# Kernel optimization log

Hardware: AMD Instinct MI355X
Metric: run time of the kernel (lower is better)

Reference implementation:

```python
import jax, jax.numpy as jnp
import numpy as np

B, L, D = 16, 1024, 512
EPS = 1e-6


def setup_inputs() -> dict:
    key = jax.random.key(0)
    ks = jax.random.split(key, 12)
    inp = {
        'q': jax.random.normal(ks[0], (B, L, D), jnp.float32),
        'k': jax.random.normal(ks[1], (B, L, D), jnp.float32),
        'v': jax.random.normal(ks[2], (B, L, D), jnp.float32),
        'inputs_lengths': jax.random.randint(ks[3], (B,), 1, L + 1),
        'distance_matrix': jax.random.uniform(ks[4], (B, L, L), jnp.float32),
        'Wq': jax.random.normal(ks[5], (D, D), jnp.float32) / np.sqrt(D),
        'Wk': jax.random.normal(ks[6], (D, D), jnp.float32) / np.sqrt(D),
        'Wv': jax.random.normal(ks[7], (D, D), jnp.float32) / np.sqrt(D),
        'Wqt': jax.random.normal(ks[8], (D, D), jnp.float32) / np.sqrt(D),
        'Wkt': jax.random.normal(ks[9], (D, D), jnp.float32) / np.sqrt(D),
        'Wfc': jax.random.normal(ks[10], (D, D), jnp.float32) / np.sqrt(D),
        'gamma': jnp.ones((D,), jnp.float32),
        'beta': jnp.zeros((D,), jnp.float32),
    }
    return inp


def reference(q, k, v, inputs_lengths, distance_matrix, Wq, Wk, Wv, Wqt, Wkt, Wfc, gamma, beta):
    temperature = jnp.asarray(D, q.dtype) ** 0.5
    residual = q
    # projections (torch Linear: x @ W.T)
    qp = jnp.einsum('bld,ed->ble', q, Wq)
    kp = jnp.einsum('bld,ed->ble', k, Wk)
    vp = jnp.einsum('bld,ed->ble', v, Wv)
    qt = jnp.einsum('bld,ed->ble', q, Wqt)
    kt = jnp.einsum('bld,ed->ble', k, Wkt)
    # distance-weighted time features: [B,L,L] @ [B,L,D]
    qt = jnp.einsum('blm,bmd->bld', distance_matrix, qt)
    kt = jnp.einsum('blm,bmd->bld', distance_matrix, kt)
    # scores: content + distance term
    attn = jnp.einsum('bld,bmd->blm', qp / temperature, kp)
    attn = attn + jnp.einsum('bld,bmd->blm', qt / temperature, kt)
    # pad_zero_masking: zero out key positions beyond each sequence length
    mask = (jnp.arange(L)[None, :] < inputs_lengths[:, None]).astype(attn.dtype)  # [B, L]
    mask = mask[:, None, :]  # [B, 1, L] broadcast over query dim
    attn = jnp.tanh(attn * mask) * mask
    out = jnp.einsum('blm,bmd->bld', attn, vp)
    out = jnp.einsum('bld,ed->ble', out, Wfc) + residual
    # LayerNorm(eps=1e-6)
    mu = jnp.mean(out, axis=-1, keepdims=True)
    var = jnp.mean((out - mu) ** 2, axis=-1, keepdims=True)
    out = (out - mu) * jax.lax.rsqrt(var + EPS) * gamma + beta
    return (out, attn)
```

## Files before the change

kernel.cpp:

```cpp
#include <hip/hip_runtime.h>
#include <math.h>

#define LL 1024
#define DD 512
#define NB 16

typedef __attribute__((ext_vector_type(8))) short bf16x8;
typedef __attribute__((ext_vector_type(4))) float f32x4;
typedef unsigned short u16;
typedef unsigned int u32;
typedef const __attribute__((address_space(1))) void* gptr_t;
typedef __attribute__((address_space(3))) void* sptr_t;

static const long NLD = (long)NB * LL * DD;
static const long NLL = (long)NB * LL * LL;

__device__ __forceinline__ u16 f2bf(float x) {
  u32 u = __float_as_uint(x);
  u += 0x7fffu + ((u >> 16) & 1u);
  return (u16)(u >> 16);
}
__device__ __forceinline__ float bf2f(u16 h) {
  return __uint_as_float((u32)h << 16);
}

__device__ __forceinline__ int xcd_chunk16(int flat) {
  const int j = flat >> 3;
  return ((j >> 4) << 7) + ((flat & 7) << 4) + (j & 15);
}

__global__ __launch_bounds__(256) void k_split3(
    const float* __restrict__ q, const float* __restrict__ k,
    const float* __restrict__ v, u16* __restrict__ qh, u16* __restrict__ ql,
    u16* __restrict__ kh, u16* __restrict__ kl, u16* __restrict__ vh) {
  const int z = blockIdx.z;
  const float* x = (z == 0) ? q : (z == 1) ? k : v;
  u16* hi = (z == 0) ? qh : (z == 1) ? kh : vh;
  u16* lo = (z == 0) ? ql : kl;
  const long stride = (long)gridDim.x * 1024;
  for (long i = ((long)blockIdx.x * 256 + threadIdx.x) * 4; i < NLD;
       i += stride) {
    const float4 vv = *(const float4*)(x + i);
    ushort4 h;
    h.x = f2bf(vv.x);
    h.y = f2bf(vv.y);
    h.z = f2bf(vv.z);
    h.w = f2bf(vv.w);
    *(ushort4*)(hi + i) = h;
    if (z < 2) {
      ushort4 s;
      s.x = f2bf(vv.x - bf2f(h.x));
      s.y = f2bf(vv.y - bf2f(h.y));
      s.z = f2bf(vv.z - bf2f(h.z));
      s.w = f2bf(vv.w - bf2f(h.w));
      *(ushort4*)(lo + i) = s;
    }
  }
}

__global__ __launch_bounds__(256) void k_splitd(const float* __restrict__ x,
                                                u16* __restrict__ hi,
                                                u16* __restrict__ lo) {
  const long stride = (long)gridDim.x * 1024;
  for (long i = ((long)blockIdx.x * 256 + threadIdx.x) * 4; i < NLL;
       i += stride) {
    const float4 v = *(const float4*)(x + i);
    ushort4 h, s;
    h.x = f2bf(v.x);
    h.y = f2bf(v.y);
    h.z = f2bf(v.z);
    h.w = f2bf(v.w);
    s.x = f2bf(v.x - bf2f(h.x));
    s.y = f2bf(v.y - bf2f(h.y));
    s.z = f2bf(v.z - bf2f(h.z));
    s.w = f2bf(v.w - bf2f(h.w));
    *(ushort4*)(hi + i) = h;
    *(ushort4*)(lo + i) = s;
  }
}

__global__ __launch_bounds__(256) void k_splitw(
    const float* __restrict__ Wq, const float* __restrict__ Wk,
    const float* __restrict__ Wv, const float* __restrict__ Wfc,
    const float* __restrict__ Wqt, const float* __restrict__ Wkt,
    u16* __restrict__ Wq_h, u16* __restrict__ Wk_h, u16* __restrict__ Wv_h,
    u16* __restrict__ Wfc_h, u16* __restrict__ Wqt_h,
    u16* __restrict__ Wqt_l, u16* __restrict__ Wkt_h,
    u16* __restrict__ Wkt_l) {
  const int z = blockIdx.z;
  const float* x;
  u16 *hi, *lo = nullptr;
  switch (z) {
    case 0: x = Wq; hi = Wq_h; break;
    case 1: x = Wk; hi = Wk_h; break;
    case 2: x = Wv; hi = Wv_h; break;
    case 3: x = Wfc; hi = Wfc_h; break;
    case 4: x = Wqt; hi = Wqt_h; lo = Wqt_l; break;
    default: x = Wkt; hi = Wkt_h; lo = Wkt_l; break;
  }
  const long i = ((long)blockIdx.x * 256 + threadIdx.x) * 4;
  const float4 v = *(const float4*)(x + i);
  ushort4 h;
  h.x = f2bf(v.x);
  h.y = f2bf(v.y);
  h.z = f2bf(v.z);
  h.w = f2bf(v.w);
  *(ushort4*)(hi + i) = h;
  if (z >= 4) {
    ushort4 s;
    s.x = f2bf(v.x - bf2f(h.x));
    s.y = f2bf(v.y - bf2f(h.y));
    s.z = f2bf(v.z - bf2f(h.z));
    s.w = f2bf(v.w - bf2f(h.w));
    *(ushort4*)(lo + i) = s;
  }
}

template <int NISS>
__device__ __forceinline__ void stage_tile(const u16* __restrict__ G, long ld,
                                           int row0, int k0, char* lds, int w,
                                           int l) {
#pragma unroll
  for (int i = 0; i < NISS; ++i) {
    const int off = i * 4096 + w * 1024 + l * 16;
    const int r = off >> 6;
    const int cp = (off >> 4) & 3;
    const int c = cp ^ ((r >> 1) & 3);
    __builtin_amdgcn_global_load_lds(
        (gptr_t)(G + (long)(row0 + r) * ld + k0 + c * 8),
        (sptr_t)(lds + i * 4096 + w * 1024), 16, 0, 0);
  }
}

__device__ __forceinline__ bf16x8 read_frag(const char* lds, int r, int ks) {
  const int cp = ks ^ ((r >> 1) & 3);
  return *(const bf16x8*)(lds + r * 64 + cp * 16);
}

__device__ __forceinline__ void core_plain(const u16* __restrict__ A, long lda,
                                           const u16* __restrict__ B, long ldb,
                                           int K, int bm, int bn, char* smem,
                                           f32x4 acc[4][4]) {
  const int tid = threadIdx.x, w = tid >> 6, l = tid & 63;
  const int wm = (w >> 1) * 64, wn = (w & 1) * 64;
  const int fr = l & 15, ks = l >> 4;
  char* As = smem;
  char* Bs = smem + 8192;
  for (int k0 = 0; k0 < K; k0 += 32) {
    stage_tile<2>(A, lda, bm, k0, As, w, l);
    stage_tile<2>(B, ldb, bn, k0, Bs, w, l);
    __syncthreads();
    bf16x8 af[4], bg[4];
#pragma unroll
    for (int i = 0; i < 4; ++i) {
      af[i] = read_frag(As, wm + i * 16 + fr, ks);
      bg[i] = read_frag(Bs, wn + i * 16 + fr, ks);
    }
#pragma unroll
    for (int mi = 0; mi < 4; ++mi)
#pragma unroll
      for (int ni = 0; ni < 4; ++ni)
        acc[mi][ni] = __builtin_amdgcn_mfma_f32_16x16x32_bf16(
            af[mi], bg[ni], acc[mi][ni], 0, 0, 0);
    __syncthreads();
  }
}

__device__ __forceinline__ void core_split(
    const u16* __restrict__ Ah, const u16* __restrict__ Al, long lda,
    const u16* __restrict__ Bh, const u16* __restrict__ Bl, long ldb, int K,
    int bm, int bn, char* smem, f32x4 acc[4][4]) {
  const int tid = threadIdx.x, w = tid >> 6, l = tid & 63;
  const int wm = (w >> 1) * 64, wn = (w & 1) * 64;
  const int fr = l & 15, ks = l >> 4;
  char* Ash = smem;
  char* Bsh = smem + 8192;
  char* Asl = smem + 16384;
  char* Bsl = smem + 24576;
  for (int k0 = 0; k0 < K; k0 += 32) {
    stage_tile<2>(Ah, lda, bm, k0, Ash, w, l);
    stage_tile<2>(Bh, ldb, bn, k0, Bsh, w, l);
    stage_tile<2>(Al, lda, bm, k0, Asl, w, l);
    stage_tile<2>(Bl, ldb, bn, k0, Bsl, w, l);
    __syncthreads();
    bf16x8 ah[4], bh[4];
#pragma unroll
    for (int i = 0; i < 4; ++i) {
      ah[i] = read_frag(Ash, wm + i * 16 + fr, ks);
      bh[i] = read_frag(Bsh, wn + i * 16 + fr, ks);
    }
#pragma unroll
    for (int mi = 0; mi < 4; ++mi)
#pragma unroll
      for (int ni = 0; ni < 4; ++ni)
        acc[mi][ni] = __builtin_amdgcn_mfma_f32_16x16x32_bf16(
            ah[mi], bh[ni], acc[mi][ni], 0, 0, 0);
    bf16x8 bl[4];
#pragma unroll
    for (int ni = 0; ni < 4; ++ni)
      bl[ni] = read_frag(Bsl, wn + ni * 16 + fr, ks);
#pragma unroll
    for (int mi = 0; mi < 4; ++mi)
#pragma unroll
      for (int ni = 0; ni < 4; ++ni)
        acc[mi][ni] = __builtin_amdgcn_mfma_f32_16x16x32_bf16(
            ah[mi], bl[ni], acc[mi][ni], 0, 0, 0);
    bf16x8 al[4];
#pragma unroll
    for (int mi = 0; mi < 4; ++mi)
      al[mi] = read_frag(Asl, wm + mi * 16 + fr, ks);
#pragma unroll
    for (int mi = 0; mi < 4; ++mi)
#pragma unroll
      for (int ni = 0; ni < 4; ++ni)
        acc[mi][ni] = __builtin_amdgcn_mfma_f32_16x16x32_bf16(
            al[mi], bh[ni], acc[mi][ni], 0, 0, 0);
    __syncthreads();
  }
}

#define EPI_PROLOG()                                       \
  const int tid = threadIdx.x, w = tid >> 6, l = tid & 63; \
  const int wm = (w >> 1) * 64, wn = (w & 1) * 64;         \
  const int fr = l & 15, ks = l >> 4;

__device__ __forceinline__ int scan_batches(const int* __restrict__ lens,
                                            int e, int mult, int* loc,
                                            int* rem) {
  for (int i = 0; i < NB; ++i) {
    const int c = mult * ((lens[i] + 127) >> 7);
    if (e < c) {
      *loc = e;
      return i;
    }
    e -= c;
  }
  *rem = e;
  return -1;
}

__global__ __launch_bounds__(256, 3) void k_proj_p(
    const u16* __restrict__ q_hi, const u16* __restrict__ k_hi,
    const u16* __restrict__ v_hi, const u16* __restrict__ Wq_h,
    const u16* __restrict__ Wk_h, const u16* __restrict__ Wv_h,
    const int* __restrict__ lens, u16* __restrict__ qp, u16* __restrict__ kp,
    u16* __restrict__ vp) {
  const int flat = xcd_chunk16(blockIdx.x);
  const u16 *A, *B;
  u16* C;
  int bm, bn;
  if (flat < 512) {
    A = q_hi;
    B = Wq_h;
    C = qp;
    bm = (flat >> 2) * 128;
    bn = (flat & 3) * 128;
  } else {
    int loc, rem;
    int b = scan_batches(lens, flat - 512, 4, &loc, &rem);
    if (b >= 0) {
      A = k_hi;
      B = Wk_h;
      C = kp;
    } else {
      b = scan_batches(lens, rem, 4, &loc, &rem);
      if (b < 0) return;
      A = v_hi;
      B = Wv_h;
      C = vp;
    }
    bm = b * 1024 + (loc >> 2) * 128;
    bn = (loc & 3) * 128;
  }
  __shared__ __align__(16) char smem[16384];
  f32x4 acc[4][4] = {};
  core_plain(A, DD, B, DD, DD, bm, bn, smem, acc);
  EPI_PROLOG()
#pragma unroll
  for (int mi = 0; mi < 4; ++mi) {
    const int R0 = bm + wm + mi * 16 + ks * 4;
#pragma unroll
    for (int ni = 0; ni < 4; ++ni) {
      const int col = bn + wn + ni * 16 + fr;
#pragma unroll
      for (int j = 0; j < 4; ++j)
        C[(long)(R0 + j) * DD + col] = f2bf(acc[mi][ni][j]);
    }
  }
}

__global__ __launch_bounds__(256, 2) void k_proj_t(
    const u16* __restrict__ q_hi, const u16* __restrict__ q_lo,
    const u16* __restrict__ k_hi, const u16* __restrict__ k_lo,
    const u16* __restrict__ Wqt_h, const u16* __restrict__ Wqt_l,
    const u16* __restrict__ Wkt_h, const u16* __restrict__ Wkt_l,
    u16* __restrict__ qT_h, u16* __restrict__ qT_l, u16* __restrict__ kT_h,
    u16* __restrict__ kT_l) {
  const int sel = blockIdx.z;
  const u16* Ah = sel ? k_hi : q_hi;
  const u16* Al = sel ? k_lo : q_lo;
  const u16* Bh = sel ? Wkt_h : Wqt_h;
  const u16* Bl = sel ? Wkt_l : Wqt_l;
  u16* Ch = sel ? kT_h : qT_h;
  u16* Cl = sel ? kT_l : qT_l;
  __shared__ __align__(16) char smem[32768];
  const int bm = blockIdx.y * 128, bn = blockIdx.x * 128;
  f32x4 acc[4][4] = {};
  core_split(Ah, Al, DD, Bh, Bl, DD, DD, bm, bn, smem, acc);
  EPI_PROLOG()
  u16* tb = (u16*)smem;
  const int b = bm >> 10, lr0 = bm & 1023;
  for (int part = 0; part < 2; ++part) {
    u16* OT = part ? Cl : Ch;
    for (int half = 0; half < 2; ++half) {
      __syncthreads();
      if ((wn >> 6) == half) {
#pragma unroll
        for (int mi = 0; mi < 4; ++mi) {
          const int rloc = wm + mi * 16 + ks * 4;
#pragma unroll
          for (int ni = 0; ni < 4; ++ni) {
            const int cloc = ni * 16 + fr;
#pragma unroll
            for (int j = 0; j < 4; ++j) {
              const float x = acc[mi][ni][j];
              const u16 h = f2bf(x);
              tb[cloc * 132 + rloc + j] = part ? f2bf(x - bf2f(h)) : h;
            }
          }
        }
      }
      __syncthreads();
      const int colg0 = bn + half * 64;
#pragma unroll
      for (int it = 0; it < 8; ++it) {
        const int i = (it * 256 + tid) * 4;
        const int cl = i >> 7, rl = i & 127;
        *(ushort4*)&OT[(long)b * LL * DD + (long)(colg0 + cl) * LL + lr0 +
                       rl] = *(ushort4*)&tb[cl * 132 + rl];
      }
    }
  }
}

__global__ __launch_bounds__(256) void k_tr(const u16* __restrict__ vp,
                                            const int* __restrict__ lens,
                                            u16* __restrict__ vpT) {
  const int b = blockIdx.z;
  const int r0 = blockIdx.y * 64, c0 = blockIdx.x * 64;
  if (r0 >= lens[b]) return;
  const u16* X = vp + (long)b * LL * DD;
  u16* O = vpT + (long)b * LL * DD;
  __shared__ u16 t[64][68];
  const int tid = threadIdx.x;
#pragma unroll
  for (int i = 0; i < 16; ++i) {
    const int idx = tid + i * 256;
    t[idx >> 6][idx & 63] = X[(long)(r0 + (idx >> 6)) * DD + c0 + (idx & 63)];
  }
  __syncthreads();
#pragma unroll
  for (int i = 0; i < 16; ++i) {
    const int idx = tid + i * 256;
    const int rr = idx >> 6, cc = idx & 63;
    O[(long)(c0 + rr) * LL + r0 + cc] = t[cc][rr];
  }
}

__global__ __launch_bounds__(256, 3) void k_dist_g(
    const u16* __restrict__ dist_h, const u16* __restrict__ dist_l,
    const u16* __restrict__ qT_h, const u16* __restrict__ qT_l,
    const u16* __restrict__ kT_h, const u16* __restrict__ kT_l,
    const int* __restrict__ lens, u16* __restrict__ qt_h,
    u16* __restrict__ qt_l, u16* __restrict__ kt_h, u16* __restrict__ kt_l) {
  const int flat = xcd_chunk16(blockIdx.x);
  int b, sel, bm, bn;
  if (flat < 512) {
    sel = 0;
    b = flat >> 5;
    const int r = flat & 31;
    const int s = r >> 4, inner = r & 15;
    bm = (s * 4 + (inner & 3)) * 128;
    bn = (inner >> 2) * 128;
  } else {
    int loc, rem;
    b = scan_batches(lens, flat - 512, 4, &loc, &rem);
    if (b < 0) return;
    sel = 1;
    bm = (loc >> 2) * 128;
    bn = (loc & 3) * 128;
  }
  const u16* Ah = dist_h + (long)b * LL * LL;
  const u16* Al = dist_l + (long)b * LL * LL;
  const u16* Bh = (sel ? kT_h : qT_h) + (long)b * LL * DD;
  const u16* Bl = (sel ? kT_l : qT_l) + (long)b * LL * DD;
  u16* Oh = (sel ? kt_h : qt_h) + (long)b * LL * DD;
  u16* Ol = (sel ? kt_l : qt_l) + (long)b * LL * DD;
  __shared__ __align__(16) char smem[32768];
  f32x4 acc[4][4] = {};
  core_split(Ah, Al, LL, Bh, Bl, LL, LL, bm, bn, smem, acc);
  EPI_PROLOG()
#pragma unroll
  for (int mi = 0; mi < 4; ++mi) {
    const int R0 = bm + wm + mi * 16 + ks * 4;
#pragma unroll
    for (int ni = 0; ni < 4; ++ni) {
      const int col = bn + wn + ni * 16 + fr;
#pragma unroll
      for (int j = 0; j < 4; ++j) {
        const long idx = (long)(R0 + j) * DD + col;
        const float x = acc[mi][ni][j];
        const u16 h = f2bf(x);
        Oh[idx] = h;
        Ol[idx] = f2bf(x - bf2f(h));
      }
    }
  }
}

__global__ __launch_bounds__(256, 3) void k_score(
    const u16* __restrict__ qp, const u16* __restrict__ kp,
    const u16* __restrict__ qt_h, const u16* __restrict__ qt_l,
    const u16* __restrict__ kt_h, const u16* __restrict__ kt_l,
    const int* __restrict__ lens, float* __restrict__ attnF,
    u16* __restrict__ attnB) {
  const int tid = threadIdx.x;
  int loc, rem;
  int b = scan_batches(lens, xcd_chunk16(blockIdx.x), 8, &loc, &rem);
  int bm, bn;
  if (b < 0) {
    for (int i = 0; i < NB; ++i) {
      const int nbn = (lens[i] + 127) >> 7;
      const int c = (8 - nbn) << 3;
      if (rem < c) {
        b = i;
        const int wdt = 8 - nbn;
        bm = (rem / wdt) * 128;
        bn = (nbn + rem % wdt) * 128;
        break;
      }
      rem -= c;
    }
    if (b < 0) return;
    const long baseF = (long)b * LL * LL;
    const float4 zf = make_float4(0.f, 0.f, 0.f, 0.f);
    const ushort4 zh = {0, 0, 0, 0};
    for (int i = tid; i < 4096; i += 256) {
      const int row = i >> 5, c = (i & 31) << 2;
      const long idx = baseF + (long)(bm + row) * LL + bn + c;
      *(float4*)&attnF[idx] = zf;
      *(ushort4*)&attnB[idx] = zh;
    }
    return;
  }
  const int nbn = (lens[b] + 127) >> 7;
  {
    const int S = nbn << 2;
    const int s = loc / S, inner = loc - s * S;
    bm = (s * 4 + (inner & 3)) * 128;
    bn = (inner >> 2) * 128;
  }
  const int len = lens[b];
  const long baseF = (long)b * LL * LL;
  const long od = (long)b * LL * DD;
  const u16* Ah = qt_h + od;
  const u16* Al = qt_l + od;
  const u16* Bh = kt_h + od;
  const u16* Bl = kt_l + od;
  const u16* Ap = qp + od;
  const u16* Bp = kp + od;
  __shared__ __align__(16) char smem[49152];
  char* Ash = smem;
  char* Bsh = smem + 8192;
  char* Asl = smem + 16384;
  char* Bsl = smem + 24576;
  char* Aps = smem + 32768;
  char* Bps = smem + 40960;
  const int w = tid >> 6, l = tid & 63;
  const int wm = (w >> 1) * 64, wn = (w & 1) * 64;
  const int fr = l & 15, ks = l >> 4;
  f32x4 acc[4][4] = {};
  for (int k0 = 0; k0 < DD; k0 += 32) {
    stage_tile<2>(Ah, DD, bm, k0, Ash, w, l);
    stage_tile<2>(Bh, DD, bn, k0, Bsh, w, l);
    stage_tile<2>(Al, DD, bm, k0, Asl, w, l);
    stage_tile<2>(Bl, DD, bn, k0, Bsl, w, l);
    stage_tile<2>(Ap, DD, bm, k0, Aps, w, l);
    stage_tile<2>(Bp, DD, bn, k0, Bps, w, l);
    __syncthreads();
    bf16x8 ah[4], bh[4];
#pragma unroll
    for (int i = 0; i < 4; ++i) {
      ah[i] = read_frag(Ash, wm + i * 16 + fr, ks);
      bh[i] = read_frag(Bsh, wn + i * 16 + fr, ks);
    }
#pragma unroll
    for (int mi = 0; mi < 4; ++mi)
#pragma unroll
      for (int ni = 0; ni < 4; ++ni)
        acc[mi][ni] = __builtin_amdgcn_mfma_f32_16x16x32_bf16(
            ah[mi], bh[ni], acc[mi][ni], 0, 0, 0);
    bf16x8 bl[4];
#pragma unroll
    for (int ni = 0; ni < 4; ++ni)
      bl[ni] = read_frag(Bsl, wn + ni * 16 + fr, ks);
#pragma unroll
    for (int mi = 0; mi < 4; ++mi)
#pragma unroll
      for (int ni = 0; ni < 4; ++ni)
        acc[mi][ni] = __builtin_amdgcn_mfma_f32_16x16x32_bf16(
            ah[mi], bl[ni], acc[mi][ni], 0, 0, 0);
    bf16x8 al[4];
#pragma unroll
    for (int mi = 0; mi < 4; ++mi)
      al[mi] = read_frag(Asl, wm + mi * 16 + fr, ks);
#pragma unroll
    for (int mi = 0; mi < 4; ++mi)
#pragma unroll
      for (int ni = 0; ni < 4; ++ni)
        acc[mi][ni] = __builtin_amdgcn_mfma_f32_16x16x32_bf16(
            al[mi], bh[ni], acc[mi][ni], 0, 0, 0);
    bf16x8 ap[4], bp[4];
#pragma unroll
    for (int i = 0; i < 4; ++i) {
      ap[i] = read_frag(Aps, wm + i * 16 + fr, ks);
      bp[i] = read_frag(Bps, wn + i * 16 + fr, ks);
    }
#pragma unroll
    for (int mi = 0; mi < 4; ++mi)
#pragma unroll
      for (int ni = 0; ni < 4; ++ni)
        acc[mi][ni] = __builtin_amdgcn_mfma_f32_16x16x32_bf16(
            ap[mi], bp[ni], acc[mi][ni], 0, 0, 0);
    __syncthreads();
  }
  const float invt = 0.04419417382415922f;
#pragma unroll
  for (int mi = 0; mi < 4; ++mi) {
    const int R0 = bm + wm + mi * 16 + ks * 4;
#pragma unroll
    for (int ni = 0; ni < 4; ++ni) {
      const int col = bn + wn + ni * 16 + fr;
      const float m = (col < len) ? 1.0f : 0.0f;
#pragma unroll
      for (int j = 0; j < 4; ++j) {
        const float s = tanhf(acc[mi][ni][j] * invt * m) * m;
        const long idx = baseF + (long)(R0 + j) * LL + col;
        attnF[idx] = s;
        attnB[idx] = f2bf(s);
      }
    }
  }
}

__global__ __launch_bounds__(256, 3) void k_pv(const u16* __restrict__ attnB,
                                               const u16* __restrict__ vpT,
                                               const int* __restrict__ lens,
                                               u16* __restrict__ out0) {
  const int flat = xcd_chunk16(blockIdx.x);
  const int b = flat >> 5;
  const int r = flat & 31;
  const int bm = (r >> 2) * 128, bn = (r & 3) * 128;
  const int Kt = ((lens[b] + 31) >> 5) << 5;
  __shared__ __align__(16) char smem[16384];
  f32x4 acc[4][4] = {};
  core_plain(attnB + (long)b * LL * LL, LL, vpT + (long)b * LL * DD, LL, Kt,
             bm, bn, smem, acc);
  u16* C = out0 + (long)b * LL * DD;
  EPI_PROLOG()
#pragma unroll
  for (int mi = 0; mi < 4; ++mi) {
    const int R0 = bm + wm + mi * 16 + ks * 4;
#pragma unroll
    for (int ni = 0; ni < 4; ++ni) {
      const int col = bn + wn + ni * 16 + fr;
#pragma unroll
      for (int j = 0; j < 4; ++j)
        C[(long)(R0 + j) * DD + col] = f2bf(acc[mi][ni][j]);
    }
  }
}

__global__ __launch_bounds__(256, 2) void k_fcln(
    const u16* __restrict__ out0, const u16* __restrict__ Wfc_h,
    const float* __restrict__ q, const float* __restrict__ gamma,
    const float* __restrict__ beta, float* __restrict__ outO) {
  __shared__ __align__(16) char smem[36864];
  __shared__ float red[2][64][5];
  const int tid = threadIdx.x, w = tid >> 6, l = tid & 63;
  const int wn = w * 128;
  const int fr = l & 15, ks = l >> 4;
  const int bm = blockIdx.x * 64;
  char* As = smem;
  char* Bs = smem + 4096;
  f32x4 acc[4][8] = {};
  for (int k0 = 0; k0 < DD; k0 += 32) {
    stage_tile<1>(out0, DD, bm, k0, As, w, l);
    stage_tile<8>(Wfc_h, DD, 0, k0, Bs, w, l);
    __syncthreads();
    bf16x8 af[4], bg[8];
#pragma unroll
    for (int mi = 0; mi < 4; ++mi) af[mi] = read_frag(As, mi * 16 + fr, ks);
#pragma unroll
    for (int ni = 0; ni < 8; ++ni)
      bg[ni] = read_frag(Bs, wn + ni * 16 + fr, ks);
#pragma unroll
    for (int mi = 0; mi < 4; ++mi)
#pragma unroll
      for (int ni = 0; ni < 8; ++ni)
        acc[mi][ni] = __builtin_amdgcn_mfma_f32_16x16x32_bf16(
            af[mi], bg[ni], acc[mi][ni], 0, 0, 0);
    __syncthreads();
  }
  float p1[4][4], p2[4][4];
#pragma unroll
  for (int mi = 0; mi < 4; ++mi)
#pragma unroll
    for (int j = 0; j < 4; ++j) {
      p1[mi][j] = 0.0f;
      p2[mi][j] = 0.0f;
    }
#pragma unroll
  for (int mi = 0; mi < 4; ++mi) {
    const int r = mi * 16 + ks * 4;
#pragma unroll
    for (int ni = 0; ni < 8; ++ni) {
      const int col = wn + ni * 16 + fr;
#pragma unroll
      for (int j = 0; j < 4; ++j) {
        const float val = acc[mi][ni][j] + q[(long)(bm + r + j) * DD + col];
        acc[mi][ni][j] = val;
        p1[mi][j] += val;
        p2[mi][j] += val * val;
      }
    }
  }
#pragma unroll
  for (int off = 1; off < 16; off <<= 1) {
#pragma unroll
    for (int mi = 0; mi < 4; ++mi)
#pragma unroll
      for (int j = 0; j < 4; ++j) {
        p1[mi][j] += __shfl_xor(p1[mi][j], off);
        p2[mi][j] += __shfl_xor(p2[mi][j], off);
      }
  }
  if (fr == 0) {
#pragma unroll
    for (int mi = 0; mi < 4; ++mi)
#pragma unroll
      for (int j = 0; j < 4; ++j) {
        red[0][mi * 16 + ks * 4 + j][w] = p1[mi][j];
        red[1][mi * 16 + ks * 4 + j][w] = p2[mi][j];
      }
  }
  __syncthreads();
#pragma unroll
  for (int mi = 0; mi < 4; ++mi) {
#pragma unroll
    for (int j = 0; j < 4; ++j) {
      const int r = mi * 16 + ks * 4 + j;
      const float s1 =
          red[0][r][0] + red[0][r][1] + red[0][r][2] + red[0][r][3];
      const float s2 =
          red[1][r][0] + red[1][r][1] + red[1][r][2] + red[1][r][3];
      const float mu = s1 * (1.0f / DD);
      const float rs = rsqrtf(s2 * (1.0f / DD) - mu * mu + 1e-6f);
#pragma unroll
      for (int ni = 0; ni < 8; ++ni) {
        const int col = wn + ni * 16 + fr;
        outO[(long)(bm + r) * DD + col] =
            (acc[mi][ni][j] - mu) * rs * gamma[col] + beta[col];
      }
    }
  }
}

extern "C" void kernel_launch(void* const* d_in, const int* in_sizes, int n_in,
                              void* d_out, int out_size, void* d_ws,
                              size_t ws_size, hipStream_t stream) {
  const float* q = (const float*)d_in[0];
  const float* k = (const float*)d_in[1];
  const float* v = (const float*)d_in[2];
  const int* lens = (const int*)d_in[3];
  const float* dist = (const float*)d_in[4];
  const float* Wq = (const float*)d_in[5];
  const float* Wk = (const float*)d_in[6];
  const float* Wv = (const float*)d_in[7];
  const float* Wqt = (const float*)d_in[8];
  const float* Wkt = (const float*)d_in[9];
  const float* Wfc = (const float*)d_in[10];
  const float* gamma = (const float*)d_in[11];
  const float* beta = (const float*)d_in[12];

  char* W = (char*)d_ws;
  const size_t SB = 16777216;
  u16* q_hi = (u16*)(W + 0 * SB);
  u16* q_lo = (u16*)(W + 1 * SB);
  u16* k_hi = (u16*)(W + 2 * SB);
  u16* k_lo = (u16*)(W + 3 * SB);
  u16* v_hi = (u16*)(W + 4 * SB);
  u16* dist_h = (u16*)(W + 5 * SB);
  u16* dist_l = (u16*)(W + 7 * SB);
  u16* qp_bf = (u16*)(W + 9 * SB);
  u16* kp_bf = (u16*)(W + 10 * SB);
  u16* vp_bf = (u16*)(W + 11 * SB);
  u16* qT_h = (u16*)(W + 16 * SB);
  u16* qT_l = (u16*)(W + 17 * SB);
  u16* kT_h = (u16*)(W + 18 * SB);
  u16* kT_l = (u16*)(W + 19 * SB);
  char* WB = W + 20 * SB;
  const size_t WS = 524288;
  u16* Wq_h = (u16*)(WB + 0 * WS);
  u16* Wk_h = (u16*)(WB + 1 * WS);
  u16* Wv_h = (u16*)(WB + 2 * WS);
  u16* Wfc_h = (u16*)(WB + 3 * WS);
  u16* Wqt_h = (u16*)(WB + 4 * WS);
  u16* Wqt_l = (u16*)(WB + 5 * WS);
  u16* Wkt_h = (u16*)(WB + 6 * WS);
  u16* Wkt_l = (u16*)(WB + 7 * WS);
  u16* qt_h = q_hi;
  u16* qt_l = q_lo;
  u16* kt_h = k_hi;
  u16* kt_l = k_lo;
  u16* vpT = v_hi;
  u16* attnB = dist_h;
  u16* out0 = qp_bf;

  float* outO = (float*)d_out;
  float* attnF = outO + NLD;

  dim3 blk(256);
  k_split3<<<dim3(1024, 1, 3), blk, 0, stream>>>(q, k, v, q_hi, q_lo, k_hi,
                                                 k_lo, v_hi);
  k_splitd<<<4096, blk, 0, stream>>>(dist, dist_h, dist_l);
  k_splitw<<<dim3(256, 1, 6), blk, 0, stream>>>(Wq, Wk, Wv, Wfc, Wqt, Wkt,
                                                Wq_h, Wk_h, Wv_h, Wfc_h,
                                                Wqt_h, Wqt_l, Wkt_h, Wkt_l);

  k_proj_p<<<1536, blk, 0, stream>>>(q_hi, k_hi, v_hi, Wq_h, Wk_h, Wv_h, lens,
                                     qp_bf, kp_bf, vp_bf);
  k_proj_t<<<dim3(4, 128, 2), blk, 0, stream>>>(q_hi, q_lo, k_hi, k_lo, Wqt_h,
                                                Wqt_l, Wkt_h, Wkt_l, qT_h,
                                                qT_l, kT_h, kT_l);
  k_tr<<<dim3(8, 16, 16), blk, 0, stream>>>(vp_bf, lens, vpT);
  k_dist_g<<<1024, blk, 0, stream>>>(dist_h, dist_l, qT_h, qT_l, kT_h, kT_l,
                                     lens, qt_h, qt_l, kt_h, kt_l);
  k_score<<<1024, blk, 0, stream>>>(qp_bf, kp_bf, qt_h, qt_l, kt_h, kt_l,
                                    lens, attnF, attnB);
  k_pv<<<512, blk, 0, stream>>>(attnB, vpT, lens, out0);
  k_fcln<<<256, blk, 0, stream>>>(out0, Wfc_h, q, gamma, beta, outO);
}
```

Baseline: 392.4 us.

## Widen distance GEMM tiles to 128x256 to halve A-tile restaging

```diff
diff --git a/kernel.cpp b/kernel.cpp
--- a/kernel.cpp
+++ b/kernel.cpp
@@ -219,9 +219,71 @@
   }
 }
 
+__device__ __forceinline__ void core_split_w(
+    const u16* __restrict__ Ah, const u16* __restrict__ Al, long lda,
+    const u16* __restrict__ Bh, const u16* __restrict__ Bl, long ldb, int K,
+    int bm, int bn, char* smem, f32x4 acc[4][8]) {
+  const int tid = threadIdx.x, w = tid >> 6, l = tid & 63;
+  const int wm = (w >> 1) * 64, wn = (w & 1) * 128;
+  const int fr = l & 15, ks = l >> 4;
+  char* Ash = smem;
+  char* Asl = smem + 8192;
+  char* Bsh = smem + 16384;
+  char* Bsl = smem + 32768;
+  for (int k0 = 0; k0 < K; k0 += 32) {
+    stage_tile<2>(Ah, lda, bm, k0, Ash, w, l);
+    stage_tile<2>(Al, lda, bm, k0, Asl, w, l);
+    stage_tile<4>(Bh, ldb, bn, k0, Bsh, w, l);
+    stage_tile<4>(Bl, ldb, bn, k0, Bsl, w, l);
+    __syncthreads();
+    bf16x8 ah[4], al[4];
+#pragma unroll
+    for (int mi = 0; mi < 4; ++mi) {
+      ah[mi] = read_frag(Ash, wm + mi * 16 + fr, ks);
+      al[mi] = read_frag(Asl, wm + mi * 16 + fr, ks);
+    }
+#pragma unroll
+    for (int hf = 0; hf < 2; ++hf) {
+      const int base = wn + hf * 64;
+      bf16x8 bh[4];
+#pragma unroll
+      for (int ni = 0; ni < 4; ++ni)
+        bh[ni] = read_frag(Bsh, base + ni * 16 + fr, ks);
+#pragma unroll
+      for (int mi = 0; mi < 4; ++mi)
+#pragma unroll
+        for (int ni = 0; ni < 4; ++ni)
+          acc[mi][hf * 4 + ni] = __builtin_amdgcn_mfma_f32_16x16x32_bf16(
+              ah[mi], bh[ni], acc[mi][hf * 4 + ni], 0, 0, 0);
+#pragma unroll
+      for (int mi = 0; mi < 4; ++mi)
+#pragma unroll
+        for (int ni = 0; ni < 4; ++ni)
+          acc[mi][hf * 4 + ni] = __builtin_amdgcn_mfma_f32_16x16x32_bf16(
+              al[mi], bh[ni], acc[mi][hf * 4 + ni], 0, 0, 0);
+      bf16x8 bl[4];
+#pragma unroll
+      for (int ni = 0; ni < 4; ++ni)
+        bl[ni] = read_frag(Bsl, base + ni * 16 + fr, ks);
+#pragma unroll
+      for (int mi = 0; mi < 4; ++mi)
+#pragma unroll
+        for (int ni = 0; ni < 4; ++ni)
+          acc[mi][hf * 4 + ni] = __builtin_amdgcn_mfma_f32_16x16x32_bf16(
+              ah[mi], bl[ni], acc[mi][hf * 4 + ni], 0, 0, 0);
+    }
+    __syncthreads();
+  }
+}
+
 #define EPI_PROLOG()                                       \
   const int tid = threadIdx.x, w = tid >> 6, l = tid & 63; \
   const int wm = (w >> 1) * 64, wn = (w & 1) * 64;         \
+  const int fr = l & 15, ks = l >> 4;
+
+#define EPI_PROLOG_W()                                     \
+  const int tid = threadIdx.x, w = tid >> 6, l = tid & 63; \
+  const int wm = (w >> 1) * 64, wn = (w & 1) * 128;        \
   const int fr = l & 15, ks = l >> 4;
 
 __device__ __forceinline__ int scan_batches(const int* __restrict__ lens,
@@ -367,7 +429,7 @@
   }
 }
 
-__global__ __launch_bounds__(256, 3) void k_dist_g(
+__global__ __launch_bounds__(256, 2) void k_dist_g(
     const u16* __restrict__ dist_h, const u16* __restrict__ dist_l,
     const u16* __restrict__ qT_h, const u16* __restrict__ qT_l,
     const u16* __restrict__ kT_h, const u16* __restrict__ kT_l,
@@ -375,20 +437,19 @@
     u16* __restrict__ qt_l, u16* __restrict__ kt_h, u16* __restrict__ kt_l) {
   const int flat = xcd_chunk16(blockIdx.x);
   int b, sel, bm, bn;
-  if (flat < 512) {
+  if (flat < 256) {
     sel = 0;
-    b = flat >> 5;
-    const int r = flat & 31;
-    const int s = r >> 4, inner = r & 15;
-    bm = (s * 4 + (inner & 3)) * 128;
-    bn = (inner >> 2) * 128;
+    b = flat >> 4;
+    const int r = flat & 15;
+    bm = (r >> 1) * 128;
+    bn = (r & 1) * 256;
   } else {
     int loc, rem;
-    b = scan_batches(lens, flat - 512, 4, &loc, &rem);
+    b = scan_batches(lens, flat - 256, 2, &loc, &rem);
     if (b < 0) return;
     sel = 1;
-    bm = (loc >> 2) * 128;
-    bn = (loc & 3) * 128;
+    bm = (loc >> 1) * 128;
+    bn = (loc & 1) * 256;
   }
   const u16* Ah = dist_h + (long)b * LL * LL;
   const u16* Al = dist_l + (long)b * LL * LL;
@@ -396,15 +457,15 @@
   const u16* Bl = (sel ? kT_l : qT_l) + (long)b * LL * DD;
   u16* Oh = (sel ? kt_h : qt_h) + (long)b * LL * DD;
   u16* Ol = (sel ? kt_l : qt_l) + (long)b * LL * DD;
-  __shared__ __align__(16) char smem[32768];
-  f32x4 acc[4][4] = {};
-  core_split(Ah, Al, LL, Bh, Bl, LL, LL, bm, bn, smem, acc);
-  EPI_PROLOG()
+  __shared__ __align__(16) char smem[49152];
+  f32x4 acc[4][8] = {};
+  core_split_w(Ah, Al, LL, Bh, Bl, LL, LL, bm, bn, smem, acc);
+  EPI_PROLOG_W()
 #pragma unroll
   for (int mi = 0; mi < 4; ++mi) {
     const int R0 = bm + wm + mi * 16 + ks * 4;
 #pragma unroll
-    for (int ni = 0; ni < 4; ++ni) {
+    for (int ni = 0; ni < 8; ++ni) {
       const int col = bn + wn + ni * 16 + fr;
 #pragma unroll
       for (int j = 0; j < 4; ++j) {
@@ -744,8 +805,8 @@
                                                 Wqt_l, Wkt_h, Wkt_l, qT_h,
                                                 qT_l, kT_h, kT_l);
   k_tr<<<dim3(8, 16, 16), blk, 0, stream>>>(vp_bf, lens, vpT);
-  k_dist_g<<<1024, blk, 0, stream>>>(dist_h, dist_l, qT_h, qT_l, kT_h, kT_l,
-                                     lens, qt_h, qt_l, kt_h, kt_l);
+  k_dist_g<<<512, blk, 0, stream>>>(dist_h, dist_l, qT_h, qT_l, kT_h, kT_l,
+                                    lens, qt_h, qt_l, kt_h, kt_l);
   k_score<<<1024, blk, 0, stream>>>(qp_bf, kp_bf, qt_h, qt_l, kt_h, kt_l,
                                     lens, attnF, attnB);
   k_pv<<<512, blk, 0, stream>>>(attnB, vpT, lens, out0);
```

Result: slower. 404.2 us (+3.0%).
